# Optimization experiments

Hardware: AMD Instinct MI355X
Metric: run time of the kernel (lower is better)

## Reference

```python
import jax, jax.numpy as jnp
import numpy as np

DIM = 384
HEADS = 12
WIN = (7, 7)
N = WIN[0] * WIN[1]
B = 4096
NW = 64  # number of windows sharing one mask


def _relative_position_index(win):
    wh, ww = win
    coords = np.stack(np.meshgrid(np.arange(wh), np.arange(ww), indexing='ij'))  # (2,wh,ww)
    flat = coords.reshape(2, -1)                                                 # (2, N)
    rel = flat[:, :, None] - flat[:, None, :]                                    # (2, N, N)
    rel = rel.transpose(1, 2, 0).astype(np.int64)
    rel[:, :, 0] += wh - 1
    rel[:, :, 1] += ww - 1
    rel[:, :, 0] *= 2 * ww - 1
    return jnp.asarray(rel.sum(-1), dtype=jnp.int32)                             # (N, N)


def setup_inputs() -> dict:
    key = jax.random.key(0)
    ks = jax.random.split(key, 7)
    std = 0.02
    return {
        'x': jax.random.normal(ks[0], (B, N, DIM), jnp.float32),
        'mask': jax.random.normal(ks[1], (NW, N, N), jnp.float32),
        'qkv_w': jax.random.normal(ks[2], (3 * DIM, DIM), jnp.float32) * std,
        'qkv_b': jnp.zeros((3 * DIM,), jnp.float32),
        'bias_table': jax.random.normal(ks[3], ((2 * WIN[0] - 1) * (2 * WIN[1] - 1), HEADS), jnp.float32) * std,
        'proj_w': jax.random.normal(ks[4], (DIM, DIM), jnp.float32) * std,
        'proj_b': jnp.zeros((DIM,), jnp.float32),
        'rel_idx': _relative_position_index(WIN),
    }


def reference(x, mask, qkv_w, qkv_b, bias_table, proj_w, proj_b, rel_idx):
    B_, n, c = x.shape
    h = HEADS
    d = c // h
    scale = d ** -0.5

    qkv = x @ qkv_w.T + qkv_b                                  # (B_, N, 3C)
    qkv = qkv.reshape(B_, n, 3, h, d).transpose(2, 0, 3, 1, 4)  # (3, B_, H, N, D)
    q, k, v = qkv[0], qkv[1], qkv[2]

    attn = jnp.einsum('bhnd,bhmd->bhnm', q, k) * scale          # (B_, H, N, N)

    bias = bias_table[rel_idx]                                  # (N, N, H)
    attn = attn + bias.transpose(2, 0, 1)[None]                 # add (1, H, N, N)

    nW = mask.shape[0]
    attn = attn.reshape(B_ // nW, nW, h, n, n) + mask[None, :, None]
    attn = attn.reshape(B_, h, n, n)

    attn = jax.nn.softmax(attn, axis=-1)
    out = jnp.einsum('bhnm,bhmd->bhnd', attn, v)                # (B_, H, N, D)
    out = out.transpose(0, 2, 1, 3).reshape(B_, n, c)
    return out @ proj_w.T + proj_b
```

## Files before the change

kernel.cpp:

```cpp
#include <hip/hip_runtime.h>

typedef __bf16 bf16;
typedef __bf16 bf16x4 __attribute__((ext_vector_type(4)));
typedef __bf16 bf16x8 __attribute__((ext_vector_type(8)));
typedef float f32x4 __attribute__((ext_vector_type(4)));
typedef float f32x16 __attribute__((ext_vector_type(16)));
typedef int i32x2 __attribute__((ext_vector_type(2)));
typedef unsigned int u32;

#define DIMC 384
#define NHEADS 12
#define NTOK 49
#define NWINB 4096
#define MROWS (NWINB*NTOK)

#define MFMA32(A,B,C) __builtin_amdgcn_mfma_f32_32x32x16_bf16(A,B,C,0,0,0)

#define GLOAD16(gsrc, lbase) \
  __builtin_amdgcn_global_load_lds( \
      (const __attribute__((address_space(1))) u32*)(gsrc), \
      (__attribute__((address_space(3))) u32*)(lbase), 16, 0, 0)

__global__ __launch_bounds__(256) void k_convert(const float4* __restrict__ in,
                                                 bf16x4* __restrict__ out, int n4) {
  int stride = gridDim.x * blockDim.x;
  for (int i = blockIdx.x * blockDim.x + threadIdx.x; i < n4; i += stride) {
    float4 v = in[i];
    bf16x4 o;
    o[0] = (bf16)v.x; o[1] = (bf16)v.y; o[2] = (bf16)v.z; o[3] = (bf16)v.w;
    out[i] = o;
  }
}

__global__ __launch_bounds__(256) void k_biasT(const float* __restrict__ table,
                                               const int* __restrict__ rel,
                                               float* __restrict__ outp) {
  int i = blockIdx.x * 256 + threadIdx.x;
  if (i < NHEADS * NTOK * NTOK) {
    int h = i / (NTOK * NTOK), r2 = i - h * (NTOK * NTOK);
    int key = r2 / NTOK, q = r2 - key * NTOK;
    outp[i] = table[rel[q * NTOK + key] * NHEADS + h];
  }
}

__global__ __launch_bounds__(256) void k_maskT(const float* __restrict__ mask,
                                               float* __restrict__ outp) {
  int i = blockIdx.x * 256 + threadIdx.x;
  if (i < 64 * NTOK * NTOK) {
    int w = i / (NTOK * NTOK), r2 = i - w * (NTOK * NTOK);
    int key = r2 / NTOK, q = r2 - key * NTOK;
    outp[i] = mask[(w * NTOK + q) * NTOK + key];
  }
}

template <int MODE>
__global__ __launch_bounds__(256) void k_gemm(const bf16* __restrict__ A,
                                              const bf16* __restrict__ Bw,
                                              const float* __restrict__ bias,
                                              bf16* __restrict__ oQ, bf16* __restrict__ oK,
                                              bf16* __restrict__ oV, float* __restrict__ oP) {
  __shared__ __align__(16) bf16 lA[2][128 * 64];
  __shared__ __align__(16) bf16 lB[2][128 * 64];
  const int t = threadIdx.x;
  const int l = t & 63;
  const int wv = t >> 6;
  const int wr = wv >> 1, wc = wv & 1;

  const u32 NXB = MODE == 0 ? 9 : 3;
  const u32 nwg = NXB * (MROWS / 128);
  u32 lin = blockIdx.y * gridDim.x + blockIdx.x;
  u32 logical = (lin & 7) * (nwg >> 3) + (lin >> 3);
  const int n0 = (int)(logical % NXB) * 128;
  const int m0 = (int)(logical / NXB) * 128;

  const int lr = l & 15, lg = l >> 4;

  const int srow = wv * 32 + (l >> 3);
  const int scolb = (l & 7) * 16;

  f32x4 acc[4][4] = {};

  int scolA[4];
#pragma unroll
  for (int i = 0; i < 4; ++i) {
    int row = srow + i * 8;
    scolA[i] = (scolb ^ ((row & 7) << 4)) >> 1;
  }

#define STAGE(BUF, K0)                                                            \
  {                                                                               \
    _Pragma("unroll") for (int i = 0; i < 4; ++i) {                               \
      int row = srow + i * 8;                                                     \
      GLOAD16(&A[(size_t)(m0 + row) * DIMC + (K0) + scolA[i]],                    \
              &lA[BUF][wv * 2048 + i * 512]);                                     \
      GLOAD16(&Bw[(size_t)(n0 + row) * DIMC + (K0) + scolA[i]],                   \
              &lB[BUF][wv * 2048 + i * 512]);                                     \
    }                                                                             \
  }

  STAGE(0, 0);

#pragma unroll
  for (int tt = 0; tt < 6; ++tt) {
    const int cur = tt & 1;
    if (tt > 0) __builtin_amdgcn_s_barrier();
    if (tt < 5) {
      STAGE(cur ^ 1, (tt + 1) * 64);
      asm volatile("s_waitcnt vmcnt(8)" ::: "memory");
    } else {
      asm volatile("s_waitcnt vmcnt(0)" ::: "memory");
    }
    __builtin_amdgcn_s_barrier();

#pragma unroll
    for (int kk = 0; kk < 64; kk += 32) {
      bf16x8 af[4], bfv[4];
#pragma unroll
      for (int f = 0; f < 4; ++f) {
        int row = wr * 64 + f * 16 + lr;
        int cb = (kk + lg * 8) * 2;
        af[f] = *reinterpret_cast<const bf16x8*>(
            &lA[cur][row * 64 + ((cb ^ ((row & 7) << 4)) >> 1)]);
      }
#pragma unroll
      for (int f = 0; f < 4; ++f) {
        int row = wc * 64 + f * 16 + lr;
        int cb = (kk + lg * 8) * 2;
        bfv[f] = *reinterpret_cast<const bf16x8*>(
            &lB[cur][row * 64 + ((cb ^ ((row & 7) << 4)) >> 1)]);
      }
#pragma unroll
      for (int fm = 0; fm < 4; ++fm)
#pragma unroll
        for (int fn = 0; fn < 4; ++fn)
          acc[fm][fn] = __builtin_amdgcn_mfma_f32_16x16x32_bf16(af[fm], bfv[fn], acc[fm][fn], 0, 0, 0);
    }
  }
#undef STAGE

#pragma unroll
  for (int fm = 0; fm < 4; ++fm) {
#pragma unroll
    for (int fn = 0; fn < 4; ++fn) {
      int c = n0 + wc * 64 + fn * 16 + lr;
      float bc = bias[c];
#pragma unroll
      for (int r = 0; r < 4; ++r) {
        int m = m0 + wr * 64 + fm * 16 + lg * 4 + r;
        float v = acc[fm][fn][r] + bc;
        if (MODE == 0) {
          int b = m / 49, n = m - b * 49;
          int which = c / 384;
          int rem = c - which * 384;
          int h = rem >> 5, d = rem & 31;
          bf16* dst = which == 0 ? oQ : (which == 1 ? oK : oV);
          dst[((b * 12 + h) * 49 + n) * 32 + d] = (bf16)v;
        } else {
          oP[m * 384 + c] = v;
        }
      }
    }
  }
}

__global__ __launch_bounds__(256, 4) void k_attn(const bf16* __restrict__ Q,
                                                 const bf16* __restrict__ K,
                                                 const bf16* __restrict__ V,
                                                 const float* __restrict__ biasT,
                                                 const float* __restrict__ maskT,
                                                 bf16* __restrict__ H) {
  __shared__ __align__(16) bf16 Vl[4][32 * 72];
  const int t = threadIdx.x, l = t & 63, wv = t >> 6;
  const int p = blockIdx.x * 4 + wv;
  const int b = p / 12, h = p - b * 12;
  const int w = b & 63;
  const size_t base = (size_t)p * (49 * 32);
  const int c = l & 31, b5 = l >> 5;
  bf16* vl = Vl[wv];

  {
    bf16x4 z = {};
    for (int i = l; i < 128; i += 64) {
      int d = i >> 2, kq = 48 + (i & 3) * 4;
      *reinterpret_cast<bf16x4*>(&vl[d * 72 + kq]) = z;
    }
  }
  for (int i = l; i < 392; i += 64) {
    int key = i >> 3, dc = (i & 7) * 4;
    bf16x4 vv = *reinterpret_cast<const bf16x4*>(&V[base + key * 32 + dc]);
#pragma unroll
    for (int j = 0; j < 4; ++j) vl[(dc + j) * 72 + key] = vv[j];
  }

  bf16x8 kf[2][2], qf[2][2];
#pragma unroll
  for (int f = 0; f < 2; ++f) {
    int row = f * 32 + c; if (row > 48) row = 48;
#pragma unroll
    for (int kd = 0; kd < 2; ++kd) {
      kf[f][kd] = *reinterpret_cast<const bf16x8*>(&K[base + row * 32 + kd * 16 + b5 * 8]);
      qf[f][kd] = *reinterpret_cast<const bf16x8*>(&Q[base + row * 32 + kd * 16 + b5 * 8]);
    }
  }

  const float scale = 0.17677669529663689f;
  const float* bT = biasT + h * 2401;
  const float* mT = maskT + w * 2401;

#pragma unroll
  for (int fn = 0; fn < 2; ++fn) {
    f32x16 s0 = {}, s1 = {};
    s0 = MFMA32(kf[0][0], qf[fn][0], s0);
    s0 = MFMA32(kf[0][1], qf[fn][1], s0);
    s1 = MFMA32(kf[1][0], qf[fn][0], s1);
    s1 = MFMA32(kf[1][1], qf[fn][1], s1);

    int q = fn * 32 + c;
    int qc = q > 48 ? 48 : q;

    float vals[32];
    float vmax = -1e30f;
#pragma unroll
    for (int fm = 0; fm < 2; ++fm) {
#pragma unroll
      for (int r = 0; r < 16; ++r) {
        int key = fm * 32 + (r & 3) + 8 * (r >> 2) + 4 * b5;
        float sv = fm ? s1[r] : s0[r];
        float v;
        if (key < 49) {
          float cm = bT[key * 49 + qc] + mT[key * 49 + qc];
          v = fmaf(sv, scale, cm);
        } else {
          v = -1e30f;
        }
        vals[fm * 16 + r] = v;
        vmax = fmaxf(vmax, v);
      }
    }
    vmax = fmaxf(vmax, __shfl_xor(vmax, 32));
    float sum = 0.f;
#pragma unroll
    for (int i = 0; i < 32; ++i) {
      float e = __expf(vals[i] - vmax);
      vals[i] = e;
      sum += e;
    }
    sum += __shfl_xor(sum, 32);
    float inv = 1.f / sum;

    f32x16 o = {};
#pragma unroll
    for (int kk = 0; kk < 4; ++kk) {
      int ib = (kk >> 1) * 16 + 8 * (kk & 1);
      union { bf16 hh[2]; u32 u; } cv;
      u32 A0, A1, B0, B1;
      cv.hh[0] = (bf16)(vals[ib + 0] * inv); cv.hh[1] = (bf16)(vals[ib + 1] * inv); A0 = cv.u;
      cv.hh[0] = (bf16)(vals[ib + 2] * inv); cv.hh[1] = (bf16)(vals[ib + 3] * inv); A1 = cv.u;
      cv.hh[0] = (bf16)(vals[ib + 4] * inv); cv.hh[1] = (bf16)(vals[ib + 5] * inv); B0 = cv.u;
      cv.hh[0] = (bf16)(vals[ib + 6] * inv); cv.hh[1] = (bf16)(vals[ib + 7] * inv); B1 = cv.u;
      i32x2 sw0 = __builtin_amdgcn_permlane32_swap((int)A0, (int)B0, false, false);
      i32x2 sw1 = __builtin_amdgcn_permlane32_swap((int)A1, (int)B1, false, false);
      union { u32 d[4]; bf16x8 v8; } pa;
      pa.d[0] = (u32)sw0[0]; pa.d[1] = (u32)sw1[0];
      pa.d[2] = (u32)sw0[1]; pa.d[3] = (u32)sw1[1];
      bf16x8 vf = *reinterpret_cast<const bf16x8*>(&vl[c * 72 + kk * 16 + b5 * 8]);
      o = MFMA32(pa.v8, vf, o);
    }

#pragma unroll
    for (int r = 0; r < 16; ++r) {
      int qrow = fn * 32 + (r & 3) + 8 * (r >> 2) + 4 * b5;
      if (qrow < 49)
        H[((size_t)b * 49 + qrow) * 384 + h * 32 + c] = (bf16)o[r];
    }
  }
}

extern "C" void kernel_launch(void* const* d_in, const int* in_sizes, int n_in,
                              void* d_out, int out_size, void* d_ws, size_t ws_size,
                              hipStream_t stream) {
  const float* x     = (const float*)d_in[0];
  const float* mask  = (const float*)d_in[1];
  const float* qkvw  = (const float*)d_in[2];
  const float* qkvb  = (const float*)d_in[3];
  const float* btab  = (const float*)d_in[4];
  const float* projw = (const float*)d_in[5];
  const float* projb = (const float*)d_in[6];
  const int*   rel   = (const int*)d_in[7];
  float* out = (float*)d_out;

  const size_t NELEM = (size_t)MROWS * DIMC;
  char* ws = (char*)d_ws;
  bf16*  xb    = (bf16*)ws;
  bf16*  vb    = (bf16*)(ws + 154140672);
  float* biasT = (float*)(ws + 308281344);
  bf16*  wqkv  = (bf16*)(ws + 308396800);
  float* maskT = (float*)(ws + 308396800);
  bf16*  wproj = (bf16*)(ws + 309281536);
  bf16* qb = (bf16*)d_out;
  bf16* kb = qb + NELEM;

  k_convert<<<2048, 256, 0, stream>>>((const float4*)x, (bf16x4*)xb, (int)(NELEM / 4));
  k_convert<<<432, 256, 0, stream>>>((const float4*)qkvw, (bf16x4*)wqkv, 3 * DIMC * DIMC / 4);
  k_convert<<<144, 256, 0, stream>>>((const float4*)projw, (bf16x4*)wproj, DIMC * DIMC / 4);
  k_biasT<<<(NHEADS * NTOK * NTOK + 255) / 256, 256, 0, stream>>>(btab, rel, biasT);

  k_gemm<0><<<dim3(1152 / 128, MROWS / 128), 256, 0, stream>>>(xb, wqkv, qkvb, qb, kb, vb, nullptr);
  k_maskT<<<(64 * NTOK * NTOK + 255) / 256, 256, 0, stream>>>(mask, maskT);
  k_attn<<<(NWINB * NHEADS) / 4, 256, 0, stream>>>(qb, kb, vb, biasT, maskT, xb);
  k_gemm<1><<<dim3(384 / 128, MROWS / 128), 256, 0, stream>>>(xb, wproj, projb, nullptr, nullptr, nullptr, out);
}
```

Before: 843.3 us.

## Store QKV row-major and shrink GEMM M-tile to 64 rows

The QKV GEMM epilogue now writes Q, K and V in plain row-major (token, 384) layout instead of the scattered per-head (b,h,n,d) layout, and the attention kernel reads each head with a 384-element row stride. Both GEMMs switch to a 64x128 tile, which doubles the number of workgroups and lowers per-block LDS and accumulator usage. The aim is contiguous epilogue stores without per-element division, plus more parallelism. The cost is that attention now reads K, Q and V with a stride, and the smaller tile reuses each B load less.

```diff
diff --git a/kernel.cpp b/kernel.cpp
--- a/kernel.cpp
+++ b/kernel.cpp
@@ -59,7 +59,7 @@
                                               const float* __restrict__ bias,
                                               bf16* __restrict__ oQ, bf16* __restrict__ oK,
                                               bf16* __restrict__ oV, float* __restrict__ oP) {
-  __shared__ __align__(16) bf16 lA[2][128 * 64];
+  __shared__ __align__(16) bf16 lA[2][64 * 64];
   __shared__ __align__(16) bf16 lB[2][128 * 64];
   const int t = threadIdx.x;
   const int l = t & 63;
@@ -67,33 +67,32 @@
   const int wr = wv >> 1, wc = wv & 1;
 
   const u32 NXB = MODE == 0 ? 9 : 3;
-  const u32 nwg = NXB * (MROWS / 128);
+  const u32 nwg = NXB * (MROWS / 64);
   u32 lin = blockIdx.y * gridDim.x + blockIdx.x;
   u32 logical = (lin & 7) * (nwg >> 3) + (lin >> 3);
   const int n0 = (int)(logical % NXB) * 128;
-  const int m0 = (int)(logical / NXB) * 128;
+  const int m0 = (int)(logical / NXB) * 64;
 
   const int lr = l & 15, lg = l >> 4;
 
-  const int srow = wv * 32 + (l >> 3);
+  const int srowA = wv * 16 + (l >> 3);
+  const int srowB = wv * 32 + (l >> 3);
   const int scolb = (l & 7) * 16;
 
-  f32x4 acc[4][4] = {};
-
-  int scolA[4];
-#pragma unroll
-  for (int i = 0; i < 4; ++i) {
-    int row = srow + i * 8;
-    scolA[i] = (scolb ^ ((row & 7) << 4)) >> 1;
-  }
+  f32x4 acc[2][4] = {};
 
 #define STAGE(BUF, K0)                                                            \
   {                                                                               \
+    _Pragma("unroll") for (int i = 0; i < 2; ++i) {                               \
+      int row = srowA + i * 8;                                                    \
+      int sc = (scolb ^ ((row & 7) << 4)) >> 1;                                   \
+      GLOAD16(&A[(size_t)(m0 + row) * DIMC + (K0) + sc],                          \
+              &lA[BUF][wv * 1024 + i * 512]);                                     \
+    }                                                                             \
     _Pragma("unroll") for (int i = 0; i < 4; ++i) {                               \
-      int row = srow + i * 8;                                                     \
-      GLOAD16(&A[(size_t)(m0 + row) * DIMC + (K0) + scolA[i]],                    \
-              &lA[BUF][wv * 2048 + i * 512]);                                     \
-      GLOAD16(&Bw[(size_t)(n0 + row) * DIMC + (K0) + scolA[i]],                   \
+      int row = srowB + i * 8;                                                    \
+      int sc = (scolb ^ ((row & 7) << 4)) >> 1;                                   \
+      GLOAD16(&Bw[(size_t)(n0 + row) * DIMC + (K0) + sc],                         \
               &lB[BUF][wv * 2048 + i * 512]);                                     \
     }                                                                             \
   }
@@ -106,7 +105,7 @@
     if (tt > 0) __builtin_amdgcn_s_barrier();
     if (tt < 5) {
       STAGE(cur ^ 1, (tt + 1) * 64);
-      asm volatile("s_waitcnt vmcnt(8)" ::: "memory");
+      asm volatile("s_waitcnt vmcnt(6)" ::: "memory");
     } else {
       asm volatile("s_waitcnt vmcnt(0)" ::: "memory");
     }
@@ -114,10 +113,10 @@
 
 #pragma unroll
     for (int kk = 0; kk < 64; kk += 32) {
-      bf16x8 af[4], bfv[4];
-#pragma unroll
-      for (int f = 0; f < 4; ++f) {
-        int row = wr * 64 + f * 16 + lr;
+      bf16x8 af[2], bfv[4];
+#pragma unroll
+      for (int f = 0; f < 2; ++f) {
+        int row = wr * 32 + f * 16 + lr;
         int cb = (kk + lg * 8) * 2;
         af[f] = *reinterpret_cast<const bf16x8*>(
             &lA[cur][row * 64 + ((cb ^ ((row & 7) << 4)) >> 1)]);
@@ -130,7 +129,7 @@
             &lB[cur][row * 64 + ((cb ^ ((row & 7) << 4)) >> 1)]);
       }
 #pragma unroll
-      for (int fm = 0; fm < 4; ++fm)
+      for (int fm = 0; fm < 2; ++fm)
 #pragma unroll
         for (int fn = 0; fn < 4; ++fn)
           acc[fm][fn] = __builtin_amdgcn_mfma_f32_16x16x32_bf16(af[fm], bfv[fn], acc[fm][fn], 0, 0, 0);
@@ -138,29 +137,34 @@
   }
 #undef STAGE
 
-#pragma unroll
-  for (int fm = 0; fm < 4; ++fm) {
-#pragma unroll
-    for (int fn = 0; fn < 4; ++fn) {
-      int c = n0 + wc * 64 + fn * 16 + lr;
-      float bc = bias[c];
+  const int cbase = n0 + wc * 64;
+  const bf16* dummy;
+  bf16* dst;
+  int col0;
+  if (MODE == 0) {
+    int which = cbase / 384;
+    dst = which == 0 ? oQ : (which == 1 ? oK : oV);
+    col0 = cbase - which * 384;
+  }
+#pragma unroll
+  for (int fn = 0; fn < 4; ++fn) {
+    int c = cbase + fn * 16 + lr;
+    float bc = bias[c];
+#pragma unroll
+    for (int fm = 0; fm < 2; ++fm) {
 #pragma unroll
       for (int r = 0; r < 4; ++r) {
-        int m = m0 + wr * 64 + fm * 16 + lg * 4 + r;
+        int m = m0 + wr * 32 + fm * 16 + lg * 4 + r;
         float v = acc[fm][fn][r] + bc;
         if (MODE == 0) {
-          int b = m / 49, n = m - b * 49;
-          int which = c / 384;
-          int rem = c - which * 384;
-          int h = rem >> 5, d = rem & 31;
-          bf16* dst = which == 0 ? oQ : (which == 1 ? oK : oV);
-          dst[((b * 12 + h) * 49 + n) * 32 + d] = (bf16)v;
+          dst[(size_t)m * 384 + col0 + fn * 16 + lr] = (bf16)v;
         } else {
-          oP[m * 384 + c] = v;
+          oP[(size_t)m * 384 + c] = v;
         }
       }
     }
   }
+  (void)dummy;
 }
 
 __global__ __launch_bounds__(256, 4) void k_attn(const bf16* __restrict__ Q,
@@ -174,7 +178,7 @@
   const int p = blockIdx.x * 4 + wv;
   const int b = p / 12, h = p - b * 12;
   const int w = b & 63;
-  const size_t base = (size_t)p * (49 * 32);
+  const size_t rbase = (size_t)b * 49 * 384 + h * 32;
   const int c = l & 31, b5 = l >> 5;
   bf16* vl = Vl[wv];
 
@@ -187,7 +191,7 @@
   }
   for (int i = l; i < 392; i += 64) {
     int key = i >> 3, dc = (i & 7) * 4;
-    bf16x4 vv = *reinterpret_cast<const bf16x4*>(&V[base + key * 32 + dc]);
+    bf16x4 vv = *reinterpret_cast<const bf16x4*>(&V[rbase + (size_t)key * 384 + dc]);
 #pragma unroll
     for (int j = 0; j < 4; ++j) vl[(dc + j) * 72 + key] = vv[j];
   }
@@ -198,8 +202,8 @@
     int row = f * 32 + c; if (row > 48) row = 48;
 #pragma unroll
     for (int kd = 0; kd < 2; ++kd) {
-      kf[f][kd] = *reinterpret_cast<const bf16x8*>(&K[base + row * 32 + kd * 16 + b5 * 8]);
-      qf[f][kd] = *reinterpret_cast<const bf16x8*>(&Q[base + row * 32 + kd * 16 + b5 * 8]);
+      kf[f][kd] = *reinterpret_cast<const bf16x8*>(&K[rbase + (size_t)row * 384 + kd * 16 + b5 * 8]);
+      qf[f][kd] = *reinterpret_cast<const bf16x8*>(&Q[rbase + (size_t)row * 384 + kd * 16 + b5 * 8]);
     }
   }
 
@@ -305,8 +309,8 @@
   k_convert<<<144, 256, 0, stream>>>((const float4*)projw, (bf16x4*)wproj, DIMC * DIMC / 4);
   k_biasT<<<(NHEADS * NTOK * NTOK + 255) / 256, 256, 0, stream>>>(btab, rel, biasT);
 
-  k_gemm<0><<<dim3(1152 / 128, MROWS / 128), 256, 0, stream>>>(xb, wqkv, qkvb, qb, kb, vb, nullptr);
+  k_gemm<0><<<dim3(9, MROWS / 64), 256, 0, stream>>>(xb, wqkv, qkvb, qb, kb, vb, nullptr);
   k_maskT<<<(64 * NTOK * NTOK + 255) / 256, 256, 0, stream>>>(mask, maskT);
   k_attn<<<(NWINB * NHEADS) / 4, 256, 0, stream>>>(qb, kb, vb, biasT, maskT, xb);
-  k_gemm<1><<<dim3(384 / 128, MROWS / 128), 256, 0, stream>>>(xb, wproj, projb, nullptr, nullptr, nullptr, out);
-}
+  k_gemm<1><<<dim3(3, MROWS / 64), 256, 0, stream>>>(xb, wproj, projb, nullptr, nullptr, nullptr, out);
+}
```

New measurement: 889.9 us. 5.5% more time.
